# Kernel optimization log

Measured on AMD Instinct MI355X. Metric: run time of the kernel, lower is better.

## Reference

```python
import jax, jax.numpy as jnp
import numpy as np

EPS = 1e-5
C = 128
B = 16384
SYMBIOTIC = 4.0
NUM_PARENTS = 16
CHILDREN_PER_PARENT = 7


def _inverse(v):
    # torch: sort -> rank -> reversed rank -> gather sorted values
    idx0 = np.argsort(v, kind='stable')
    value = v[idx0]
    idx1 = np.argsort(idx0, kind='stable')  # ranks
    idx2 = v.shape[0] - 1 - idx1
    return value[idx2]


def _build_stats():
    counts = np.floor(50000.0 * 0.97 ** np.arange(C)) + 1.0  # long-tailed
    N = counts.sum()
    weight = (N / counts).astype(np.float32)
    prior = np.eye(C, dtype=np.float32)
    for p in range(NUM_PARENTS):
        ch = NUM_PARENTS + CHILDREN_PER_PARENT * p + np.arange(CHILDREN_PER_PARENT)
        prior[p, ch] = 1.0
    prior_me = (prior == 0).astype(np.float32)          # 1 - prior, keep only exact 1s
    prior_ms = prior - np.eye(C, dtype=np.float32)      # prior (0/1) minus eye
    v1_sig = np.log(N / counts - 1.0 + EPS).astype(np.float32)
    v2_sig = _inverse(v1_sig).astype(np.float32)
    v1_sm = np.log(counts / N + EPS).astype(np.float32)
    v2_sm = _inverse(v1_sm).astype(np.float32)
    return weight, prior_me, prior_ms, v1_sig, v2_sig, v1_sm, v2_sm


def setup_inputs() -> dict:
    key = jax.random.key(0)
    k1, k2 = jax.random.split(key)
    weight, prior_me, prior_ms, v1s, v2s, v1m, v2m = _build_stats()
    logits = 0.5 * jax.random.normal(k1, (12, B, C), dtype=jnp.float32)
    target = (jax.random.uniform(k2, (B, C)) < 0.1).astype(jnp.float32)
    return {
        'logits': logits, 'target': target,
        'weight': jnp.asarray(weight),
        'prior_me': jnp.asarray(prior_me), 'prior_ms': jnp.asarray(prior_ms),
        'v1_sigmoid': jnp.asarray(v1s), 'v2_sigmoid': jnp.asarray(v2s),
        'v1_softmax': jnp.asarray(v1m), 'v2_softmax': jnp.asarray(v2m),
    }


def reference(logits, target, weight, prior_me, prior_ms,
              v1_sigmoid, v2_sigmoid, v1_softmax, v2_softmax):
    zero = jnp.zeros_like(v1_sigmoid)
    # experts 0-5: sigmoid variants (long-tailed / balanced / inversed, twice)
    sig_shift = jnp.stack([zero, v1_sigmoid, v1_sigmoid - v2_sigmoid] * 2)  # [6,C]
    a_sig = jax.nn.sigmoid(logits[:6] - sig_shift[:, None, :])
    # experts 6-11: local-softmax variants
    sm_shift = jnp.stack([zero, v1_softmax, v1_softmax - v2_softmax] * 2)   # [6,C]
    e = jnp.exp(logits[6:] + sm_shift[:, None, :])                          # [6,B,C]
    denom = jnp.einsum('ebc,cd->ebd', e, prior_me) + e
    a_sm = e / (denom + EPS)
    acti = jnp.clip(jnp.concatenate([a_sig, a_sm], axis=0), EPS, 1.0 - EPS)  # [12,B,C]
    # weighted BCE per expert, summed
    bce = -weight * (target * jnp.log(acti) + (1.0 - target) * jnp.log(1.0 - acti))
    loss = jnp.sum(jnp.mean(bce, axis=(1, 2)))
    # symbiotic regularizer on experts 3,4,5,9,10,11
    row_sum = jnp.sum(prior_ms, axis=1)                 # [C]
    n_nz = jnp.sum(row_sum > 0).astype(acti.dtype)
    bsz = acti.shape[1]

    def symb(a):  # a: [B,C] activated logits
        def step(acc, xs):
            mask_row, parent = xs                       # [C], [B]
            term = jnp.log1p(jnp.exp(a - parent[:, None]))  # [B,C]
            rs = jnp.sum(mask_row)
            contrib = jnp.where(rs > 0, jnp.sum(term * mask_row) / (bsz * rs), 0.0)
            return acc + contrib, None
        total, _ = jax.lax.scan(step, jnp.float32(0.0), (prior_ms, a.T))
        return total / n_nz

    reg = jax.vmap(symb)(acti[jnp.array([3, 4, 5, 9, 10, 11])])
    return loss + SYMBIOTIC * jnp.sum(reg)
```

## Files before the change

### kernel.cpp

```cpp
#include <hip/hip_runtime.h>
#include <math.h>

#define CC 128
#define BB 16384
#define MEPS 1e-5f
#define NBLK 2048
#define PSZ ((size_t)BB * CC)


__device__ __forceinline__ float softplus1(float d) {
    const float u = d * d;
    float p = fmaf(u, 3.4722222e-4f, -5.2083333e-3f);
    p = fmaf(u, p, 0.125f);
    return fmaf(u, p, fmaf(d, 0.5f, 0.69314718f));
}

__global__ __launch_bounds__(256, 4) void mel_main(
    const float* __restrict__ logits, const float* __restrict__ target,
    const float* __restrict__ weight,
    const float* __restrict__ v1s, const float* __restrict__ v2s,
    const float* __restrict__ v1m, const float* __restrict__ v2m,
    float* __restrict__ partial)
{
    const int lane = threadIdx.x & 63;
    const int wib  = threadIdx.x >> 6;
    const int blk  = (int)blockIdx.x & (NBLK - 1);
    const int wave = blk * 4 + wib;
    const int r    = lane >> 5;
    const int c    = lane & 31;
    const size_t ro = (size_t)(wave * 2 + r) * CC;

    const float4 wt4 = ((const float4*)weight)[c];
    const float4 s1v = ((const float4*)v1s)[c];
    const float4 s2v = ((const float4*)v2s)[c];
    const float4 m1v = ((const float4*)v1m)[c];
    const float4 m2v = ((const float4*)v2m)[c];
    const float4 tv  = ((const float4*)(target + ro))[c];

    const float wt[4] = {wt4.x, wt4.y, wt4.z, wt4.w};
    const float s1[4] = {s1v.x, s1v.y, s1v.z, s1v.w};
    const float sd[4] = {s1v.x - s2v.x, s1v.y - s2v.y, s1v.z - s2v.z, s1v.w - s2v.w};
    const float m1[4] = {m1v.x, m1v.y, m1v.z, m1v.w};
    const float md[4] = {m1v.x - m2v.x, m1v.y - m2v.y, m1v.z - m2v.z, m1v.w - m2v.w};
    const float tn[4] = {1.f - tv.x, 1.f - tv.y, 1.f - tv.z, 1.f - tv.w};
    const bool  tb[4] = {tv.x > 0.5f, tv.y > 0.5f, tv.z > 0.5f, tv.w > 0.5f};

    const float childf = (c >= 4) ? 1.f : 0.f;
    int pofs[4];
    #pragma unroll
    for (int k = 0; k < 4; ++k) {
        const int ch = 4 * c + k;
        pofs[k] = (ch >= 16) ? (ch - 16) / 7 : 0;
    }

    __shared__ float lds[4][2][3][16];
    float* Lp = &lds[wib][r][0][0];

    const float* plane = logits + ro;
    float4 L0 = ((const float4*)plane)[c];
    float4 L1 = ((const float4*)(plane + PSZ))[c];
    float4 L2 = ((const float4*)(plane + 2 * PSZ))[c];
    plane += 3 * PSZ;

    float accP = 0.f;
    float accS = 0.f;
    float zsum[4] = {0.f, 0.f, 0.f, 0.f};

    #pragma unroll 1
    for (int g = 0; g < 2; ++g) {
        const float x0[4] = {L0.x, L0.y, L0.z, L0.w};
        const float x1[4] = {L1.x, L1.y, L1.z, L1.w};
        const float x2[4] = {L2.x, L2.y, L2.z, L2.w};
        L0 = ((const float4*)plane)[c];
        L1 = ((const float4*)(plane + PSZ))[c];
        L2 = ((const float4*)(plane + 2 * PSZ))[c];
        plane += 3 * PSZ;

        float av[3][4];
        #pragma unroll
        for (int si = 0; si < 3; ++si) {
            #pragma unroll
            for (int k = 0; k < 4; ++k) {
                const float x  = (si == 0) ? x0[k] : (si == 1) ? x1[k] : x2[k];
                const float sh = (si == 0) ? 0.f   : (si == 1) ? s1[k] : sd[k];
                const float z  = x - sh;
                const float ex = __expf(-z);
                accP = fmaf(wt[k], __logf(1.f + ex), accP);
                zsum[k] += z;
                if (g == 1) av[si][k] = __builtin_amdgcn_rcpf(1.f + ex);
            }
        }
        if (g == 1) {
            if (c < 4) {
                #pragma unroll
                for (int si = 0; si < 3; ++si)
                    *(float4*)(Lp + si * 16 + 4 * c) =
                        make_float4(av[si][0], av[si][1], av[si][2], av[si][3]);
            }
            #pragma unroll
            for (int si = 0; si < 3; ++si)
                #pragma unroll
                for (int k = 0; k < 4; ++k)
                    accS = fmaf(childf, softplus1(av[si][k] - Lp[si * 16 + pofs[k]]), accS);
        }
    }

    #pragma unroll 1
    for (int g = 0; g < 2; ++g) {
        const float x0[4] = {L0.x, L0.y, L0.z, L0.w};
        const float x1[4] = {L1.x, L1.y, L1.z, L1.w};
        const float x2[4] = {L2.x, L2.y, L2.z, L2.w};
        if (g == 0) {
            L0 = ((const float4*)plane)[c];
            L1 = ((const float4*)(plane + PSZ))[c];
            L2 = ((const float4*)(plane + 2 * PSZ))[c];
        }

        float ex[3][4], S[3];
        #pragma unroll
        for (int si = 0; si < 3; ++si) {
            S[si] = 0.f;
            #pragma unroll
            for (int k = 0; k < 4; ++k) {
                const float x  = (si == 0) ? x0[k] : (si == 1) ? x1[k] : x2[k];
                const float sh = (si == 0) ? 0.f   : (si == 1) ? m1[k] : md[k];
                ex[si][k] = __expf(x + sh);
                S[si] += ex[si][k];
            }
        }
        #pragma unroll
        for (int off = 16; off > 0; off >>= 1)
            #pragma unroll
            for (int si = 0; si < 3; ++si)
                S[si] += __shfl_xor(S[si], off, 64);

        if (c < 4) {
            #pragma unroll
            for (int si = 0; si < 3; ++si)
                *(float4*)(Lp + si * 16 + 4 * c) =
                    make_float4(ex[si][0], ex[si][1], ex[si][2], ex[si][3]);
        }

        #pragma unroll
        for (int si = 0; si < 3; ++si) {
            const float Sj = S[si] + MEPS;
            const float rS = __builtin_amdgcn_rcpf(Sj);
            #pragma unroll
            for (int k = 0; k < 4; ++k) {
                const float ep  = Lp[si * 16 + pofs[k]];
                const float den = Sj - childf * ep;
                float a = ex[si][k] * __builtin_amdgcn_rcpf(den);
                a = fminf(fmaxf(a, MEPS), 1.f - MEPS);
                const float arg = tb[k] ? a : 1.f - a;
                accP = fmaf(wt[k], -__logf(arg), accP);
                if (g == 1)
                    accS = fmaf(childf, softplus1(a - ep * rS), accS);
            }
        }
    }

    #pragma unroll
    for (int k = 0; k < 4; ++k)
        accP = fmaf(wt[k] * tn[k], zsum[k], accP);

    float val = accP * (1.f / ((float)BB * (float)CC))
              + accS * (4.f / (112.f * (float)BB));

    #pragma unroll
    for (int off = 32; off > 0; off >>= 1)
        val += __shfl_xor(val, off, 64);

    __shared__ float sdata[4];
    if (lane == 0) sdata[wib] = val;
    __syncthreads();
    if (threadIdx.x == 0)
        partial[blockIdx.x] = (sdata[0] + sdata[1]) + (sdata[2] + sdata[3]);
}

__global__ __launch_bounds__(256) void mel_reduce(
    const float* __restrict__ partial, float* __restrict__ out)
{
    float v = 0.f;
    #pragma unroll
    for (int i = 0; i < 2 * NBLK / 256; ++i)
        v += partial[threadIdx.x + i * 256];
    #pragma unroll
    for (int off = 32; off > 0; off >>= 1)
        v += __shfl_xor(v, off, 64);
    __shared__ float s[4];
    const int lane = threadIdx.x & 63, wib = threadIdx.x >> 6;
    if (lane == 0) s[wib] = v;
    __syncthreads();
    if (threadIdx.x == 0) out[0] = 0.5f * ((s[0] + s[1]) + (s[2] + s[3]));
}

extern "C" void kernel_launch(void* const* d_in, const int* in_sizes, int n_in,
                              void* d_out, int out_size, void* d_ws, size_t ws_size,
                              hipStream_t stream) {
    const float* logits = (const float*)d_in[0];
    const float* target = (const float*)d_in[1];
    const float* weight = (const float*)d_in[2];
    const float* v1s = (const float*)d_in[5];
    const float* v2s = (const float*)d_in[6];
    const float* v1m = (const float*)d_in[7];
    const float* v2m = (const float*)d_in[8];
    float* partial = (float*)d_ws;
    float* out = (float*)d_out;

    mel_main<<<2 * NBLK, 256, 0, stream>>>(logits, target, weight,
                                           v1s, v2s, v1m, v2m, partial);
    mel_reduce<<<1, 256, 0, stream>>>(partial, out);
}
```

Measured before the change: 187.9 us.

## Drop duplicated grid and replace per-element logs with running products

The main kernel previously ran twice as many blocks as needed. The extra blocks recomputed the same rows, and the reducer halved the sum to compensate. That launch is now cut to NBLK blocks and the halving is removed. The BCE terms also change: instead of one log per element, the kernel keeps running products of numerators and denominators for the sigmoid and softmax parts and takes four logs per lane at the end. The clamp is rewritten in a ratio form. This removes many transcendental ops, at the risk of float overflow or underflow in the products and slightly different clamping semantics.

```diff
diff --git a/kernel.cpp b/kernel.cpp
--- a/kernel.cpp
+++ b/kernel.cpp
@@ -15,7 +15,7 @@
     return fmaf(u, p, fmaf(d, 0.5f, 0.69314718f));
 }
 
-__global__ __launch_bounds__(256, 4) void mel_main(
+__global__ __launch_bounds__(256) void mel_main(
     const float* __restrict__ logits, const float* __restrict__ target,
     const float* __restrict__ weight,
     const float* __restrict__ v1s, const float* __restrict__ v2s,
@@ -24,8 +24,7 @@
 {
     const int lane = threadIdx.x & 63;
     const int wib  = threadIdx.x >> 6;
-    const int blk  = (int)blockIdx.x & (NBLK - 1);
-    const int wave = blk * 4 + wib;
+    const int wave = blockIdx.x * 4 + wib;
     const int r    = lane >> 5;
     const int c    = lane & 31;
     const size_t ro = (size_t)(wave * 2 + r) * CC;
@@ -42,7 +41,6 @@
     const float sd[4] = {s1v.x - s2v.x, s1v.y - s2v.y, s1v.z - s2v.z, s1v.w - s2v.w};
     const float m1[4] = {m1v.x, m1v.y, m1v.z, m1v.w};
     const float md[4] = {m1v.x - m2v.x, m1v.y - m2v.y, m1v.z - m2v.z, m1v.w - m2v.w};
-    const float tn[4] = {1.f - tv.x, 1.f - tv.y, 1.f - tv.z, 1.f - tv.w};
     const bool  tb[4] = {tv.x > 0.5f, tv.y > 0.5f, tv.z > 0.5f, tv.w > 0.5f};
 
     const float childf = (c >= 4) ? 1.f : 0.f;
@@ -62,9 +60,9 @@
     float4 L2 = ((const float4*)(plane + 2 * PSZ))[c];
     plane += 3 * PSZ;
 
-    float accP = 0.f;
+    float PnA[4] = {1.f, 1.f, 1.f, 1.f}, PdA[4] = {1.f, 1.f, 1.f, 1.f};
+    float PnB[4] = {1.f, 1.f, 1.f, 1.f}, PdB[4] = {1.f, 1.f, 1.f, 1.f};
     float accS = 0.f;
-    float zsum[4] = {0.f, 0.f, 0.f, 0.f};
 
     #pragma unroll 1
     for (int g = 0; g < 2; ++g) {
@@ -83,11 +81,11 @@
             for (int k = 0; k < 4; ++k) {
                 const float x  = (si == 0) ? x0[k] : (si == 1) ? x1[k] : x2[k];
                 const float sh = (si == 0) ? 0.f   : (si == 1) ? s1[k] : sd[k];
-                const float z  = x - sh;
-                const float ex = __expf(-z);
-                accP = fmaf(wt[k], __logf(1.f + ex), accP);
-                zsum[k] += z;
-                if (g == 1) av[si][k] = __builtin_amdgcn_rcpf(1.f + ex);
+                const float ex = __expf(sh - x);
+                const float d  = 1.f + ex;
+                PdA[k] *= d;
+                PnA[k] *= tb[k] ? 1.f : ex;
+                if (g == 1) av[si][k] = __builtin_amdgcn_rcpf(d);
             }
         }
         if (g == 1) {
@@ -149,19 +147,26 @@
             for (int k = 0; k < 4; ++k) {
                 const float ep  = Lp[si * 16 + pofs[k]];
                 const float den = Sj - childf * ep;
-                float a = ex[si][k] * __builtin_amdgcn_rcpf(den);
-                a = fminf(fmaxf(a, MEPS), 1.f - MEPS);
-                const float arg = tb[k] ? a : 1.f - a;
-                accP = fmaf(wt[k], -__logf(arg), accP);
-                if (g == 1)
-                    accS = fmaf(childf, softplus1(a - ep * rS), accS);
-            }
-        }
-    }
-
-    #pragma unroll
-    for (int k = 0; k < 4; ++k)
-        accP = fmaf(wt[k] * tn[k], zsum[k], accP);
+                const float e   = ex[si][k];
+                const float ec  = fmaxf(e, MEPS * den);
+                PnB[k] *= tb[k] ? ec : den - ec;
+                PdB[k] *= den;
+                if (g == 1) {
+                    const float a  = ec * __builtin_amdgcn_rcpf(den);
+                    const float ap = fmaxf(ep * rS, MEPS);
+                    accS = fmaf(childf, softplus1(a - ap), accS);
+                }
+            }
+        }
+    }
+
+    float accP = 0.f;
+    #pragma unroll
+    for (int k = 0; k < 4; ++k) {
+        const float lg = (__logf(PdA[k]) - __logf(PnA[k]))
+                       + (__logf(PdB[k]) - __logf(PnB[k]));
+        accP = fmaf(wt[k], lg, accP);
+    }
 
     float val = accP * (1.f / ((float)BB * (float)CC))
               + accS * (4.f / (112.f * (float)BB));
@@ -182,7 +187,7 @@
 {
     float v = 0.f;
     #pragma unroll
-    for (int i = 0; i < 2 * NBLK / 256; ++i)
+    for (int i = 0; i < NBLK / 256; ++i)
         v += partial[threadIdx.x + i * 256];
     #pragma unroll
     for (int off = 32; off > 0; off >>= 1)
@@ -191,7 +196,7 @@
     const int lane = threadIdx.x & 63, wib = threadIdx.x >> 6;
     if (lane == 0) s[wib] = v;
     __syncthreads();
-    if (threadIdx.x == 0) out[0] = 0.5f * ((s[0] + s[1]) + (s[2] + s[3]));
+    if (threadIdx.x == 0) out[0] = (s[0] + s[1]) + (s[2] + s[3]);
 }
 
 extern "C" void kernel_launch(void* const* d_in, const int* in_sizes, int n_in,
@@ -207,7 +212,7 @@
     float* partial = (float*)d_ws;
     float* out = (float*)d_out;
 
-    mel_main<<<2 * NBLK, 256, 0, stream>>>(logits, target, weight,
-                                           v1s, v2s, v1m, v2m, partial);
+    mel_main<<<NBLK, 256, 0, stream>>>(logits, target, weight,
+                                       v1s, v2s, v1m, v2m, partial);
     mel_reduce<<<1, 256, 0, stream>>>(partial, out);
 }
```

Result: faster. 169.3 us (-9.9%).
